# Kernel optimization log

Hardware: AMD Instinct MI355X
Metric: run time of the kernel (lower is better)

## Reference

```python
import jax, jax.numpy as jnp
import numpy as np

B, T, C = 128, 512, 1024  # batch, time (fixed by `line` buffer), channels


def fft_convolve(a, b):
    """Linear convolution via zero-padded FFT, sliced to a's length.
    a: (1, C, T) kernel, b: (B, C, T) signal. Returns (B, C, T)."""
    n = a.shape[-1]
    a_pad = jnp.pad(a, ((0, 0), (0, 0), (0, n)))
    b_pad = jnp.pad(b, ((0, 0), (0, 0), (0, n)))
    spec = jnp.fft.rfft(a_pad, axis=-1) * jnp.fft.rfft(b_pad, axis=-1)
    return jnp.fft.irfft(spec, n=2 * n, axis=-1)[..., :n]


def setup_inputs() -> dict:
    key = jax.random.key(0)
    k1, k2, k3, k4, k5 = jax.random.split(key, 5)
    bound = 1.0 / np.sqrt(C)  # nn.Linear default init range
    x = jax.random.normal(k1, (B, T, C), dtype=jnp.float32)
    W_proj = jax.random.uniform(k2, (C, C), jnp.float32, -bound, bound)
    W_values = jax.random.uniform(k3, (C, C), jnp.float32, -bound, bound)
    gain = jax.random.uniform(k4, (1, 1, C), jnp.float32, 0.01, 1.0)
    pow_ = jax.random.uniform(k5, (1, C, 1), jnp.float32, -6.0, 6.0)
    line = jnp.linspace(1.0, 0.0, T, dtype=jnp.float32)[None, None, :]  # (1,1,T)
    return {"x": x, "W_proj": W_proj, "W_values": W_values,
            "gain": gain, "pow_": pow_, "line": line}


def reference(x, W_proj, W_values, gain, pow_, line):
    # proj and values (bias-free Linears)
    h = jnp.einsum('btc,dc->btd', x, W_proj)          # (B,T,C)
    v = jnp.einsum('btc,dc->btd', h, W_values)        # (B,T,C)
    # learned power-law kernel, one decay per channel: (1,C,T)
    z = line ** (2.0 + jax.nn.sigmoid(pow_) * 100.0)
    # FFT long convolution along time
    y = fft_convolve(z, jnp.transpose(v, (0, 2, 1)))  # (B,C,T)
    y = jnp.transpose(y, (0, 2, 1))                    # (B,T,C)
    return jax.nn.relu(y * gain)
```

## Files before the change

### kernel.cpp

```cpp
#include <hip/hip_runtime.h>
#include <hip/hip_bf16.h>

#define B_ 128
#define T_ 512
#define C_ 1024

typedef __attribute__((ext_vector_type(8))) short short8;
typedef __attribute__((ext_vector_type(4))) float f32x4;

__device__ __forceinline__ unsigned short f2bf(float f){
  unsigned u; __builtin_memcpy(&u, &f, 4);
  u += 0x7FFFu + ((u >> 16) & 1u);
  return (unsigned short)(u >> 16);
}

typedef __attribute__((address_space(3))) unsigned lds_u32_t;
typedef __attribute__((address_space(1))) unsigned glb_u32_t;
typedef __attribute__((address_space(3))) char lds_char;
__device__ __forceinline__ void gload16(const void* g, void* l){
  __builtin_amdgcn_global_load_lds((const glb_u32_t*)g, (lds_u32_t*)l, 16, 0, 0);
}

__global__ void cast_f32_bf16(const float* __restrict__ in, unsigned short* __restrict__ out, long n){
  long i = (long)blockIdx.x * blockDim.x + threadIdx.x;
  long stride = (long)gridDim.x * blockDim.x;
  for (long j = i * 4; j < n; j += stride * 4){
    float4 v = *(const float4*)(in + j);
    ushort4 o; o.x = f2bf(v.x); o.y = f2bf(v.y); o.z = f2bf(v.z); o.w = f2bf(v.w);
    *(ushort4*)(out + j) = o;
  }
}

__global__ void transpose_cast(const float* __restrict__ in, unsigned short* __restrict__ out){
  __shared__ float tile[32][33];
  int c0 = blockIdx.x * 32, e0 = blockIdx.y * 32;
  int tx = threadIdx.x, ty = threadIdx.y;
  for (int r = 0; r < 32; r += 8)
    tile[ty + r][tx] = in[(size_t)(e0 + ty + r) * C_ + c0 + tx];
  __syncthreads();
  for (int r = 0; r < 32; r += 8)
    out[(size_t)(c0 + ty + r) * C_ + e0 + tx] = f2bf(tile[tx][ty + r]);
}

__global__ __launch_bounds__(256) void gemm_bt_bf16(
    const unsigned short* __restrict__ A,
    const unsigned short* __restrict__ Bt,
    unsigned short* __restrict__ Cc,
    int M, int N, int K)
{
  __shared__ short As[128 * 32];
  __shared__ short Bs[128 * 32];
  const int tid  = threadIdx.x;
  const int lane = tid & 63;
  const int wave = tid >> 6;
  const int wr = wave >> 1, wc = wave & 1;
  const int lr = lane & 15, kg = lane >> 4;
  const int m0 = blockIdx.x * 128;
  const int n0 = blockIdx.y * 128;

  f32x4 acc[4][4];
  #pragma unroll
  for (int mi = 0; mi < 4; mi++)
    #pragma unroll
    for (int ni = 0; ni < 4; ni++)
      acc[mi][ni] = (f32x4){0.f, 0.f, 0.f, 0.f};

  const int r1 = tid >> 2, ch1 = tid & 3;
  char* abase = (char*)As + (tid & ~63) * 16;
  char* bbase = (char*)Bs + (tid & ~63) * 16;

  for (int k0 = 0; k0 < K; k0 += 32){
    __syncthreads();
    gload16(A  + (size_t)(m0 + r1)      * K + k0 + ch1 * 8, abase);
    gload16(A  + (size_t)(m0 + 64 + r1) * K + k0 + ch1 * 8, abase + 4096);
    gload16(Bt + (size_t)(n0 + r1)      * K + k0 + ch1 * 8, bbase);
    gload16(Bt + (size_t)(n0 + 64 + r1) * K + k0 + ch1 * 8, bbase + 4096);
    __syncthreads();

    short8 af[4], bfr[4];
    #pragma unroll
    for (int mi = 0; mi < 4; mi++)
      af[mi] = *(const short8*)&As[(wr * 64 + mi * 16 + lr) * 32 + kg * 8];
    #pragma unroll
    for (int ni = 0; ni < 4; ni++)
      bfr[ni] = *(const short8*)&Bs[(wc * 64 + ni * 16 + lr) * 32 + kg * 8];
    #pragma unroll
    for (int mi = 0; mi < 4; mi++)
      #pragma unroll
      for (int ni = 0; ni < 4; ni++)
        acc[mi][ni] = __builtin_amdgcn_mfma_f32_16x16x32_bf16(af[mi], bfr[ni], acc[mi][ni], 0, 0, 0);
  }

  #pragma unroll
  for (int mi = 0; mi < 4; mi++)
    #pragma unroll
    for (int ni = 0; ni < 4; ni++){
      int n = n0 + wc * 64 + ni * 16 + lr;
      int mb = m0 + wr * 64 + mi * 16 + kg * 4;
      #pragma unroll
      for (int j = 0; j < 4; j++)
        Cc[(size_t)(mb + j) * N + n] = f2bf(acc[mi][ni][j]);
    }
}

#define SWZ(x) ((x) ^ ((((x) >> 7) & 3) << 4))

#define STAGE_B(kt, kh) { \
  int d_ = wv * 1024 + ln * 16; int o_ = SWZ(d_); \
  gload16(Bg + (size_t)(n0 + (o_ >> 6)) * 1024 + (kt) * 64 + (kh) * 32 + ((o_ >> 4) & 3) * 8, \
          ldsc + 65536 + ((kt) & 1) * 32768 + (kh) * 16384 + wv * 1024); \
  d_ += 8192; o_ = SWZ(d_); \
  gload16(Bg + (size_t)(n0 + (o_ >> 6)) * 1024 + (kt) * 64 + (kh) * 32 + ((o_ >> 4) & 3) * 8, \
          ldsc + 65536 + ((kt) & 1) * 32768 + (kh) * 16384 + 8192 + wv * 1024); }

#define LOADA(kt) { \
  _Pragma("unroll") for (int kh = 0; kh < 2; kh++) \
    _Pragma("unroll") for (int hf = 0; hf < 2; hf++){ \
      const float* p_ = Ag32 + (size_t)(m0 + rowA + hf * 128) * 1024 + (kt) * 64 + kh * 32 + c8 * 8; \
      areg[kh][hf][0] = *(const float4*)p_; \
      areg[kh][hf][1] = *(const float4*)(p_ + 4); } }

#define CVTWRITE(slot) { \
  _Pragma("unroll") for (int kh = 0; kh < 2; kh++) \
    _Pragma("unroll") for (int hf = 0; hf < 2; hf++){ \
      short8 w_; \
      _Pragma("unroll") for (int q = 0; q < 4; q++){ \
        w_[q]     = (short)f2bf(areg[kh][hf][0][q]); \
        w_[q + 4] = (short)f2bf(areg[kh][hf][1][q]); } \
      int d_ = wv * 1024 + ln * 16 + hf * 8192; \
      unsigned ad_ = (unsigned)(size_t)(lds3 + (slot) * 32768 + kh * 16384 + SWZ(d_)); \
      asm volatile("ds_write_b128 %0, %1" :: "v"(ad_), "v"(w_)); } }

#define MFMA4(MI) { \
  acc[MI][0] = __builtin_amdgcn_mfma_f32_16x16x32_bf16(af[MI], bfr[0], acc[MI][0], 0, 0, 0); \
  acc[MI][1] = __builtin_amdgcn_mfma_f32_16x16x32_bf16(af[MI], bfr[1], acc[MI][1], 0, 0, 0); \
  acc[MI][2] = __builtin_amdgcn_mfma_f32_16x16x32_bf16(af[MI], bfr[2], acc[MI][2], 0, 0, 0); \
  acc[MI][3] = __builtin_amdgcn_mfma_f32_16x16x32_bf16(af[MI], bfr[3], acc[MI][3], 0, 0, 0); }

#define LSTEP(N, MI) { \
  asm volatile("s_waitcnt lgkmcnt(" #N ")"); \
  __builtin_amdgcn_sched_barrier(0); \
  MFMA4(MI); }

#define KHALF(S, KHOFF) { \
  _Pragma("unroll") for (int ni = 0; ni < 4; ni++){ \
    int off = 65536 + (S) * 32768 + (KHOFF) + (wc * 64 + ni * 16 + lr) * 64 + kg * 16; \
    unsigned a_ = (unsigned)(size_t)(lds3 + SWZ(off)); \
    asm volatile("ds_read_b128 %0, %1" : "=v"(bfr[ni]) : "v"(a_)); } \
  _Pragma("unroll") for (int mi = 0; mi < 8; mi++){ \
    int off = (S) * 32768 + (KHOFF) + (wr * 128 + mi * 16 + lr) * 64 + kg * 16; \
    unsigned a_ = (unsigned)(size_t)(lds3 + SWZ(off)); \
    asm volatile("ds_read_b128 %0, %1" : "=v"(af[mi]) : "v"(a_)); } \
  __builtin_amdgcn_s_setprio(1); \
  LSTEP(7, 0) LSTEP(6, 1) LSTEP(5, 2) LSTEP(4, 3) \
  LSTEP(3, 4) LSTEP(2, 5) LSTEP(1, 6) LSTEP(0, 7) \
  __builtin_amdgcn_s_setprio(0); \
  __builtin_amdgcn_sched_barrier(0); }

__global__ __launch_bounds__(512, 2) void gemm256_fused(
    const float* __restrict__ Ag32,
    const unsigned short* __restrict__ Bg,
    unsigned short* __restrict__ vt)
{
  extern __shared__ char ldsc[];
  lds_char* lds3 = (lds_char*)ldsc;
  const int tid = threadIdx.x;
  const int ln  = tid & 63;
  const int wv  = tid >> 6;
  const int wr  = wv >> 2;
  const int wc  = wv & 3;
  const int lr  = ln & 15, kg = ln >> 4;
  const int rowA = wv * 16 + (ln >> 2);
  const int c8   = ln & 3;
  const int id  = blockIdx.x;
  const int jj  = (id & 7) * 128 + (id >> 3);
  const int n0  = (jj & 3) * 256;
  const int m0  = (jj >> 2) * 256;

  f32x4 acc[8][4];
  #pragma unroll
  for (int mi = 0; mi < 8; mi++)
    #pragma unroll
    for (int ni = 0; ni < 4; ni++)
      acc[mi][ni] = (f32x4){0.f, 0.f, 0.f, 0.f};

  float4 areg[2][2][2];

  LOADA(0);
  asm volatile("s_waitcnt vmcnt(0)");
  __builtin_amdgcn_sched_barrier(0);
  CVTWRITE(0);
  __builtin_amdgcn_sched_barrier(0);
  STAGE_B(0, 0); STAGE_B(0, 1);
  __builtin_amdgcn_sched_barrier(0);
  asm volatile("s_waitcnt lgkmcnt(0)");
  __builtin_amdgcn_sched_barrier(0);
  asm volatile("s_waitcnt vmcnt(0)");
  __builtin_amdgcn_sched_barrier(0);
  __builtin_amdgcn_s_barrier();

  short8 af[8], bfr[4];

  #pragma unroll 1
  for (int t = 0; t < 16; ++t){
    const int S = t & 1;

    if (t < 15){
      LOADA(t + 1);
      __builtin_amdgcn_sched_barrier(0);
      STAGE_B(t + 1, 0); STAGE_B(t + 1, 1);
      __builtin_amdgcn_sched_barrier(0);
    }

    KHALF(S, 0)
    KHALF(S, 16384)

    if (t < 15){
      asm volatile("s_waitcnt vmcnt(0)");
      __builtin_amdgcn_sched_barrier(0);
      CVTWRITE(S ^ 1);
      __builtin_amdgcn_sched_barrier(0);
      asm volatile("s_waitcnt lgkmcnt(0)");
      __builtin_amdgcn_sched_barrier(0);
    }
    __builtin_amdgcn_s_barrier();
  }

  #pragma unroll
  for (int mi = 0; mi < 8; mi++)
    #pragma unroll
    for (int ni = 0; ni < 4; ni++){
      int n  = n0 + wc * 64 + ni * 16 + lr;
      int mb = m0 + wr * 128 + mi * 16 + kg * 4;
      int bb = mb >> 9, t = mb & 511;
      ushort4 o;
      o.x = f2bf(acc[mi][ni][0]); o.y = f2bf(acc[mi][ni][1]);
      o.z = f2bf(acc[mi][ni][2]); o.w = f2bf(acc[mi][ni][3]);
      *(ushort4*)&vt[((size_t)n * B_ + bb) * T_ + t] = o;
    }
}

__global__ __launch_bounds__(256) void conv_mfma3(
    const unsigned short* __restrict__ vt,
    const float* __restrict__ pw,
    const float* __restrict__ line,
    const float* __restrict__ gain,
    unsigned short* __restrict__ Ybf)
{
  __shared__ short Bs[128 * 32];
  __shared__ short Ab[16 * 1280];
  __shared__ unsigned short zbuf[512];
  lds_char* ldsB = (lds_char*)Bs;
  lds_char* ldsA = (lds_char*)Ab;
  const int id  = blockIdx.x;
  const int xcd = id & 7;
  const int jj  = id >> 3;
  const int c   = xcd + ((jj >> 2) << 3);
  const int t0  = (jj & 3) << 7;
  const int tid = threadIdx.x, lane = tid & 63, wave = tid >> 6;
  const int wr = wave >> 1, wc = wave & 1, lr = lane & 15, kg = lane >> 4;
  const int K  = t0 + 128;
  const int nIter = K >> 5;
  const int nb = (t0 >> 5) + 4;

  {
    float p = pw[c];
    float e = 2.0f + 100.0f / (1.0f + expf(-p));
    for (int k = tid; k < K; k += 256){
      float lv = line[k];
      float z = (lv > 0.f) ? expf(e * logf(lv)) : 0.f;
      zbuf[k] = f2bf(z);
    }
  }
  __syncthreads();
  for (int idx = tid; idx < nb * 1280; idx += 256){
    int i = idx / 40, j = idx - i * 40;
    int d32 = i >> 5, ii = i & 31;
    int k = d32 * 32 + ii - j;
    unsigned short v = 0;
    if (j < 32 && k >= 0) v = zbuf[k];
    Ab[idx] = v;
  }

  f32x4 acc[4][4];
  #pragma unroll
  for (int mi = 0; mi < 4; mi++)
    #pragma unroll
    for (int ni = 0; ni < 4; ni++)
      acc[mi][ni] = (f32x4){0.f, 0.f, 0.f, 0.f};

  const int r1 = tid >> 2, ch1 = tid & 3;
  const size_t vbase = (size_t)c * B_ * T_;
  const unsigned adw0 = (unsigned)(size_t)(ldsB + tid * 16);
  const unsigned adw1 = adw0 + 4096;

  short8 va0 = *(const short8*)&vt[vbase + (size_t)r1 * T_        + ch1 * 8];
  short8 va1 = *(const short8*)&vt[vbase + (size_t)(64 + r1) * T_ + ch1 * 8];

  #pragma unroll 1
  for (int it = 0; it < nIter; ++it){
    const int k0 = it << 5;
    asm volatile("ds_write_b128 %0, %1" :: "v"(adw0), "v"(va0));
    asm volatile("ds_write_b128 %0, %1" :: "v"(adw1), "v"(va1));
    asm volatile("s_waitcnt lgkmcnt(0)");
    __builtin_amdgcn_sched_barrier(0);
    __builtin_amdgcn_s_barrier();

    if (it + 1 < nIter){
      va0 = *(const short8*)&vt[vbase + (size_t)r1 * T_        + k0 + 32 + ch1 * 8];
      va1 = *(const short8*)&vt[vbase + (size_t)(64 + r1) * T_ + k0 + 32 + ch1 * 8];
    }

    short8 bfr[4], afv[4];
    #pragma unroll
    for (int ni = 0; ni < 4; ni++){
      unsigned a_ = (unsigned)(size_t)(ldsB + (wc * 64 + ni * 16 + lr) * 64 + kg * 16);
      asm volatile("ds_read_b128 %0, %1" : "=v"(bfr[ni]) : "v"(a_));
    }
    const int dbase = ((t0 - k0) >> 5) + wr * 2;
    #pragma unroll
    for (int mi = 0; mi < 4; mi++){
      int d32 = dbase + (mi >> 1);
      int d32c = d32 < 0 ? 0 : d32;
      int i = ((mi & 1) << 4) + lr;
      unsigned a_ = (unsigned)(size_t)(ldsA + (d32c * 1280 + i * 40 + kg * 8) * 2);
      asm volatile("ds_read_b128 %0, %1" : "=v"(afv[mi]) : "v"(a_));
    }
    asm volatile("s_waitcnt lgkmcnt(0)");
    __builtin_amdgcn_sched_barrier(0);
    __builtin_amdgcn_s_setprio(1);
    #pragma unroll
    for (int mi = 0; mi < 4; mi++){
      if (dbase + (mi >> 1) >= 0){
        #pragma unroll
        for (int ni = 0; ni < 4; ni++)
          acc[mi][ni] = __builtin_amdgcn_mfma_f32_16x16x32_bf16(afv[mi], bfr[ni], acc[mi][ni], 0, 0, 0);
      }
    }
    __builtin_amdgcn_s_setprio(0);
    __builtin_amdgcn_sched_barrier(0);
    __builtin_amdgcn_s_barrier();
  }

  const float g = gain[c];
  #pragma unroll
  for (int mi = 0; mi < 4; mi++)
    #pragma unroll
    for (int ni = 0; ni < 4; ni++){
      int t = t0 + wr * 64 + mi * 16 + kg * 4;
      int b = wc * 64 + ni * 16 + lr;
      ushort4 o;
      o.x = f2bf(fmaxf(acc[mi][ni][0] * g, 0.f));
      o.y = f2bf(fmaxf(acc[mi][ni][1] * g, 0.f));
      o.z = f2bf(fmaxf(acc[mi][ni][2] * g, 0.f));
      o.w = f2bf(fmaxf(acc[mi][ni][3] * g, 0.f));
      *(ushort4*)&Ybf[((size_t)c * B_ + b) * T_ + t] = o;
    }
}

__global__ __launch_bounds__(256) void final_out(const unsigned short* __restrict__ Ybf,
                                                 float* __restrict__ out){
  __shared__ unsigned short tile[64][72];
  const int c0 = blockIdx.x * 64;
  const int t0 = blockIdx.y * 64;
  const int b  = blockIdx.z;
  const int tid = threadIdx.x;
  const int cr = tid >> 4;
  const int t4 = (tid & 15) * 4;
  for (int q = 0; q < 64; q += 16){
    ushort4 u = *(const ushort4*)&Ybf[((size_t)(c0 + cr + q) * B_ + b) * T_ + t0 + t4];
    *(ushort4*)&tile[cr + q][t4] = u;
  }
  __syncthreads();
  const int tr = tid >> 4;
  const int c4 = (tid & 15) * 4;
  for (int q = 0; q < 64; q += 16){
    int t = tr + q;
    float4 o;
    o.x = __uint_as_float((unsigned)tile[c4 + 0][t] << 16);
    o.y = __uint_as_float((unsigned)tile[c4 + 1][t] << 16);
    o.z = __uint_as_float((unsigned)tile[c4 + 2][t] << 16);
    o.w = __uint_as_float((unsigned)tile[c4 + 3][t] << 16);
    *(float4*)&out[((size_t)b * T_ + t0 + t) * C_ + c0 + c4] = o;
  }
}

extern "C" void kernel_launch(void* const* d_in, const int* in_sizes, int n_in,
                              void* d_out, int out_size, void* d_ws, size_t ws_size,
                              hipStream_t stream)
{
  (void)in_sizes; (void)n_in; (void)out_size; (void)ws_size;
  const float* x    = (const float*)d_in[0];
  const float* Wp   = (const float*)d_in[1];
  const float* Wv   = (const float*)d_in[2];
  const float* gain = (const float*)d_in[3];
  const float* pw   = (const float*)d_in[4];
  const float* line = (const float*)d_in[5];
  float* out = (float*)d_out;

  char* ws = (char*)d_ws;
  unsigned short* Ybf   = (unsigned short*)ws;
  unsigned short* WpT   = (unsigned short*)(ws + 134217728);
  unsigned short* Wv_bf = (unsigned short*)(ws + 134217728 + 2097152);
  unsigned short* W_f   = (unsigned short*)(ws + 134217728 + 2 * 2097152);
  unsigned short* vt    = (unsigned short*)d_out + 67108864;

  cast_f32_bf16<<<256, 256, 0, stream>>>(Wv, Wv_bf, (long)C_ * C_);
  transpose_cast<<<dim3(32, 32), dim3(32, 8), 0, stream>>>(Wp, WpT);
  gemm_bt_bf16<<<dim3(8, 8), 256, 0, stream>>>(Wv_bf, WpT, W_f, C_, C_, C_);
  gemm256_fused<<<1024, 512, 131072, stream>>>(x, W_f, vt);
  conv_mfma3<<<4096, 256, 0, stream>>>(vt, pw, line, gain, Ybf);
  final_out<<<dim3(16, 8, 128), 256, 0, stream>>>(Ybf, out);
}
```

Before: 437.9 us.

## Process full time axis per channel in one 512-thread conv block

Result: faster. 422.4 us (median of 2 runs) (-3.5%).

```diff
diff --git a/kernel.cpp b/kernel.cpp
--- a/kernel.cpp
+++ b/kernel.cpp
@@ -240,7 +240,7 @@
     }
 }
 
-__global__ __launch_bounds__(256) void conv_mfma3(
+__global__ __launch_bounds__(512) void conv_mfma4(
     const unsigned short* __restrict__ vt,
     const float* __restrict__ pw,
     const float* __restrict__ line,
@@ -252,28 +252,23 @@
   __shared__ unsigned short zbuf[512];
   lds_char* ldsB = (lds_char*)Bs;
   lds_char* ldsA = (lds_char*)Ab;
-  const int id  = blockIdx.x;
-  const int xcd = id & 7;
-  const int jj  = id >> 3;
-  const int c   = xcd + ((jj >> 2) << 3);
-  const int t0  = (jj & 3) << 7;
+  const int c   = blockIdx.x;
   const int tid = threadIdx.x, lane = tid & 63, wave = tid >> 6;
-  const int wr = wave >> 1, wc = wave & 1, lr = lane & 15, kg = lane >> 4;
-  const int K  = t0 + 128;
-  const int nIter = K >> 5;
-  const int nb = (t0 >> 5) + 4;
+  const int t0w = (wave >> 1) << 7;
+  const int bh  = wave & 1;
+  const int lr = lane & 15, kg = lane >> 4;
 
   {
     float p = pw[c];
     float e = 2.0f + 100.0f / (1.0f + expf(-p));
-    for (int k = tid; k < K; k += 256){
+    for (int k = tid; k < T_; k += 512){
       float lv = line[k];
       float z = (lv > 0.f) ? expf(e * logf(lv)) : 0.f;
       zbuf[k] = f2bf(z);
     }
   }
   __syncthreads();
-  for (int idx = tid; idx < nb * 1280; idx += 256){
+  for (int idx = tid; idx < 16 * 1280; idx += 512){
     int i = idx / 40, j = idx - i * 40;
     int d32 = i >> 5, ii = i & 31;
     int k = d32 * 32 + ii - j;
@@ -281,74 +276,72 @@
     if (j < 32 && k >= 0) v = zbuf[k];
     Ab[idx] = v;
   }
-
-  f32x4 acc[4][4];
-  #pragma unroll
-  for (int mi = 0; mi < 4; mi++)
+  __syncthreads();
+
+  f32x4 acc[8][4];
+  #pragma unroll
+  for (int mi = 0; mi < 8; mi++)
     #pragma unroll
     for (int ni = 0; ni < 4; ni++)
       acc[mi][ni] = (f32x4){0.f, 0.f, 0.f, 0.f};
 
   const int r1 = tid >> 2, ch1 = tid & 3;
   const size_t vbase = (size_t)c * B_ * T_;
-  const unsigned adw0 = (unsigned)(size_t)(ldsB + tid * 16);
-  const unsigned adw1 = adw0 + 4096;
-
-  short8 va0 = *(const short8*)&vt[vbase + (size_t)r1 * T_        + ch1 * 8];
-  short8 va1 = *(const short8*)&vt[vbase + (size_t)(64 + r1) * T_ + ch1 * 8];
+  const unsigned adw = (unsigned)(size_t)(ldsB + tid * 16);
+
+  short8 va = *(const short8*)&vt[vbase + (size_t)r1 * T_ + ch1 * 8];
 
   #pragma unroll 1
-  for (int it = 0; it < nIter; ++it){
+  for (int it = 0; it < 16; ++it){
     const int k0 = it << 5;
-    asm volatile("ds_write_b128 %0, %1" :: "v"(adw0), "v"(va0));
-    asm volatile("ds_write_b128 %0, %1" :: "v"(adw1), "v"(va1));
+    asm volatile("ds_write_b128 %0, %1" :: "v"(adw), "v"(va));
     asm volatile("s_waitcnt lgkmcnt(0)");
     __builtin_amdgcn_sched_barrier(0);
     __builtin_amdgcn_s_barrier();
 
-    if (it + 1 < nIter){
-      va0 = *(const short8*)&vt[vbase + (size_t)r1 * T_        + k0 + 32 + ch1 * 8];
-      va1 = *(const short8*)&vt[vbase + (size_t)(64 + r1) * T_ + k0 + 32 + ch1 * 8];
-    }
-
-    short8 bfr[4], afv[4];
+    if (it + 1 < 16)
+      va = *(const short8*)&vt[vbase + (size_t)r1 * T_ + k0 + 32 + ch1 * 8];
+
+    if (t0w + 128 > k0){
+      short8 bfr[4], afv[8];
+      #pragma unroll
+      for (int ni = 0; ni < 4; ni++){
+        unsigned a_ = (unsigned)(size_t)(ldsB + (bh * 64 + ni * 16 + lr) * 64 + kg * 16);
+        asm volatile("ds_read_b128 %0, %1" : "=v"(bfr[ni]) : "v"(a_));
+      }
+      const int dbase = (t0w - k0) >> 5;
+      #pragma unroll
+      for (int mi = 0; mi < 8; mi++){
+        int d32 = dbase + (mi >> 1);
+        int d32c = d32 < 0 ? 0 : d32;
+        int i = ((mi & 1) << 4) + lr;
+        unsigned a_ = (unsigned)(size_t)(ldsA + (d32c * 1280 + i * 40 + kg * 8) * 2);
+        asm volatile("ds_read_b128 %0, %1" : "=v"(afv[mi]) : "v"(a_));
+      }
+      asm volatile("s_waitcnt lgkmcnt(0)");
+      __builtin_amdgcn_sched_barrier(0);
+      __builtin_amdgcn_s_setprio(1);
+      #pragma unroll
+      for (int mi = 0; mi < 8; mi++){
+        if (dbase + (mi >> 1) >= 0){
+          #pragma unroll
+          for (int ni = 0; ni < 4; ni++)
+            acc[mi][ni] = __builtin_amdgcn_mfma_f32_16x16x32_bf16(afv[mi], bfr[ni], acc[mi][ni], 0, 0, 0);
+        }
+      }
+      __builtin_amdgcn_s_setprio(0);
+      __builtin_amdgcn_sched_barrier(0);
+    }
+    __builtin_amdgcn_s_barrier();
+  }
+
+  const float g = gain[c];
+  #pragma unroll
+  for (int mi = 0; mi < 8; mi++)
     #pragma unroll
     for (int ni = 0; ni < 4; ni++){
-      unsigned a_ = (unsigned)(size_t)(ldsB + (wc * 64 + ni * 16 + lr) * 64 + kg * 16);
-      asm volatile("ds_read_b128 %0, %1" : "=v"(bfr[ni]) : "v"(a_));
-    }
-    const int dbase = ((t0 - k0) >> 5) + wr * 2;
-    #pragma unroll
-    for (int mi = 0; mi < 4; mi++){
-      int d32 = dbase + (mi >> 1);
-      int d32c = d32 < 0 ? 0 : d32;
-      int i = ((mi & 1) << 4) + lr;
-      unsigned a_ = (unsigned)(size_t)(ldsA + (d32c * 1280 + i * 40 + kg * 8) * 2);
-      asm volatile("ds_read_b128 %0, %1" : "=v"(afv[mi]) : "v"(a_));
-    }
-    asm volatile("s_waitcnt lgkmcnt(0)");
-    __builtin_amdgcn_sched_barrier(0);
-    __builtin_amdgcn_s_setprio(1);
-    #pragma unroll
-    for (int mi = 0; mi < 4; mi++){
-      if (dbase + (mi >> 1) >= 0){
-        #pragma unroll
-        for (int ni = 0; ni < 4; ni++)
-          acc[mi][ni] = __builtin_amdgcn_mfma_f32_16x16x32_bf16(afv[mi], bfr[ni], acc[mi][ni], 0, 0, 0);
-      }
-    }
-    __builtin_amdgcn_s_setprio(0);
-    __builtin_amdgcn_sched_barrier(0);
-    __builtin_amdgcn_s_barrier();
-  }
-
-  const float g = gain[c];
-  #pragma unroll
-  for (int mi = 0; mi < 4; mi++)
-    #pragma unroll
-    for (int ni = 0; ni < 4; ni++){
-      int t = t0 + wr * 64 + mi * 16 + kg * 4;
-      int b = wc * 64 + ni * 16 + lr;
+      int t = t0w + mi * 16 + kg * 4;
+      int b = bh * 64 + ni * 16 + lr;
       ushort4 o;
       o.x = f2bf(fmaxf(acc[mi][ni][0] * g, 0.f));
       o.y = f2bf(fmaxf(acc[mi][ni][1] * g, 0.f));
@@ -409,6 +402,6 @@
   transpose_cast<<<dim3(32, 32), dim3(32, 8), 0, stream>>>(Wp, WpT);
   gemm_bt_bf16<<<dim3(8, 8), 256, 0, stream>>>(Wv_bf, WpT, W_f, C_, C_, C_);
   gemm256_fused<<<1024, 512, 131072, stream>>>(x, W_f, vt);
-  conv_mfma3<<<4096, 256, 0, stream>>>(vt, pw, line, gain, Ybf);
+  conv_mfma4<<<1024, 512, 0, stream>>>(vt, pw, line, gain, Ybf);
   final_out<<<dim3(16, 8, 128), 256, 0, stream>>>(Ybf, out);
 }
```
